# Optimization experiments

Hardware: AMD Instinct MI355X
Metric: run time of the kernel (lower is better)

## Reference

```python
import jax, jax.numpy as jnp
import numpy as np
from jax import lax

B, T, V, E, H = 256, 512, 128, 64, 256


def lstm_cell(x, h, c, Wih, Whh, bih, bhh):
    # PyTorch gate order: i, f, g, o
    gates = x @ Wih.T + h @ Whh.T + bih + bhh
    i, f, g, o = jnp.split(gates, 4, axis=-1)
    c_new = jax.nn.sigmoid(f) * c + jax.nn.sigmoid(i) * jnp.tanh(g)
    h_new = jax.nn.sigmoid(o) * jnp.tanh(c_new)
    return h_new, c_new


def setup_inputs() -> dict:
    key = jax.random.key(0)
    ks = jax.random.split(key, 16)
    s = 0.05
    emb = jax.random.normal(ks[1], (V, E), jnp.float32) * s
    emb = emb.at[0].set(0.0)  # padding_idx=0
    return {
        "x": jax.random.randint(ks[0], (B, T), 0, V),
        "emb": emb,
        "Wih_e": jax.random.normal(ks[2], (4 * H, E), jnp.float32) * s,
        "Whh_e": jax.random.normal(ks[3], (4 * H, H), jnp.float32) * s,
        "bih_e": jax.random.normal(ks[4], (4 * H,), jnp.float32) * s,
        "bhh_e": jax.random.normal(ks[5], (4 * H,), jnp.float32) * s,
        "Wq": jax.random.normal(ks[6], (H, H), jnp.float32) * s,
        "Wk": jax.random.normal(ks[7], (H, H), jnp.float32) * s,
        "v": jax.random.normal(ks[8], (H,), jnp.float32) * s,
        "Wih_d": jax.random.normal(ks[9], (4 * H, E + H), jnp.float32) * s,
        "Whh_d": jax.random.normal(ks[10], (4 * H, H), jnp.float32) * s,
        "bih_d": jax.random.normal(ks[11], (4 * H,), jnp.float32) * s,
        "bhh_d": jax.random.normal(ks[12], (4 * H,), jnp.float32) * s,
        "Wfc": jax.random.normal(ks[13], (V, H), jnp.float32) * s,
        "bfc": jax.random.normal(ks[14], (V,), jnp.float32) * s,
    }


def reference(x, emb, Wih_e, Whh_e, bih_e, bhh_e, Wq, Wk, v,
              Wih_d, Whh_d, bih_d, bhh_d, Wfc, bfc):
    Bx = x.shape[0]
    embedded = emb[x]                          # (B, T, E)  (dropout in eval mode = identity)
    emb_tbE = embedded.transpose(1, 0, 2)      # (T, B, E)

    # ---- Encoder LSTM ----
    h0 = jnp.zeros((Bx, H), embedded.dtype)
    c0 = jnp.zeros((Bx, H), embedded.dtype)

    def enc_step(carry, x_t):
        h, c = carry
        h, c = lstm_cell(x_t, h, c, Wih_e, Whh_e, bih_e, bhh_e)
        return (h, c), h

    (h_n, c_n), enc_seq = lax.scan(enc_step, (h0, c0), emb_tbE)
    enc_out = enc_seq.transpose(1, 0, 2)       # (B, T, H)

    # ---- Attention precompute ----
    keys_proj = enc_out @ Wk.T                 # (B, T, H)
    pad_mask = (x == 0)                        # (B, T)

    # ---- Decoder loop (teacher forcing) ----
    def dec_step(carry, emb_t):
        h, c = carry
        q = h @ Wq.T                                        # (B, H)
        energy = jnp.tanh(q[:, None, :] + keys_proj) @ v    # (B, T)
        energy = jnp.where(pad_mask, -1e9, energy)
        w = jax.nn.softmax(energy, axis=-1)
        context = jnp.einsum('bt,bth->bh', w, enc_out)      # (B, H)
        dec_in = jnp.concatenate([emb_t, context], axis=-1)  # (B, E+H)
        h, c = lstm_cell(dec_in, h, c, Wih_d, Whh_d, bih_d, bhh_d)
        return (h, c), h

    (h_f, c_f), dec_seq = lax.scan(dec_step, (h_n, c_n), emb_tbE)
    logits = dec_seq.transpose(1, 0, 2) @ Wfc.T + bfc       # (B, T, V)
    return logits, h_f, c_f
```

## Files before the change

kernel.cpp:

```cpp
#include <hip/hip_runtime.h>
#include <hip/hip_bf16.h>
#include <stdint.h>

#define NB 256
#define NT 512
#define NV 128
#define NE 64
#define NH 256

typedef __fp16 h2t __attribute__((ext_vector_type(2)));

__device__ __forceinline__ float lo_bf(unsigned u){ return __uint_as_float(u << 16); }
__device__ __forceinline__ float hi_bf(unsigned u){ return __uint_as_float(u & 0xffff0000u); }
__device__ __forceinline__ unsigned short f2us(float f){
  unsigned u = __float_as_uint(f);
  unsigned r = u + 0x7fffu + ((u >> 16) & 1u);
  return (unsigned short)(r >> 16);
}
__device__ __forceinline__ float sigm(float x){
  return __builtin_amdgcn_rcpf(1.f + __expf(-x));
}
__device__ __forceinline__ float ftanh(float xx){
  float a = fabsf(xx);
  a = fminf(a, 9.f);
  float e = __expf(2.f * a);
  float r = __builtin_amdgcn_rcpf(e + 1.f);
  float t = (e - 1.f) * r;
  return copysignf(t, xx);
}
__device__ __forceinline__ unsigned pkf16(float a, float b){
  h2t h = __builtin_amdgcn_cvt_pkrtz(a, b);
  unsigned u; __builtin_memcpy(&u, &h, 4); return u;
}
__device__ __forceinline__ float fdot2(unsigned a, unsigned b, float c){
#if __has_builtin(__builtin_amdgcn_fdot2)
  h2t A, B; __builtin_memcpy(&A, &a, 4); __builtin_memcpy(&B, &b, 4);
  return __builtin_amdgcn_fdot2(A, B, c, false);
#else
  h2t A, B; __builtin_memcpy(&A, &a, 4); __builtin_memcpy(&B, &b, 4);
  return c + (float)A.x*(float)B.x + (float)A.y*(float)B.y;
#endif
}

__global__ __launch_bounds__(256, 1)
void prep_kernel(const float* __restrict__ Wq, const float* __restrict__ Wfc,
                 const float* __restrict__ Wihd, const float* __restrict__ Whhd,
                 const float* __restrict__ Wihe, const float* __restrict__ Whhe,
                 const float* __restrict__ Wk,
                 unsigned* __restrict__ Wq4, unsigned* __restrict__ Wfc4,
                 unsigned* __restrict__ Wihd4, unsigned* __restrict__ Whhd4,
                 unsigned* __restrict__ Wihe4, unsigned* __restrict__ Whhe4,
                 unsigned* __restrict__ Wke4)
{
  const int blk = blockIdx.x, tid = threadIdx.x;
  if (blk < 64){
    int k2p = blk;
    #pragma unroll
    for (int l = 0; l < 2; ++l){
      int i = l*256 + tid, c = i>>1, j = i&1, k = 4*k2p + 2*j;
      Wq4[k2p*512 + i] = pkf16(Wq[c*256 + k], Wq[c*256 + k + 1]);
    }
  } else if (blk < 128){
    int k2p = blk - 64;
    int c = tid>>1, j = tid&1, k = 4*k2p + 2*j;
    Wfc4[k2p*256 + tid] = pkf16(Wfc[c*256 + k], Wfc[c*256 + k + 1]);
  } else if (blk < 208){
    int k2p = blk - 128;
    #pragma unroll
    for (int l = 0; l < 8; ++l){
      int i = l*256 + tid, g = i>>1, j = i&1, k = 4*k2p + 2*j;
      Wihd4[(size_t)k2p*2048 + i] = pkf16(Wihd[g*320 + k], Wihd[g*320 + k + 1]);
    }
  } else if (blk < 272){
    int k2p = blk - 208;
    #pragma unroll
    for (int l = 0; l < 8; ++l){
      int i = l*256 + tid, g = i>>1, j = i&1, k = 4*k2p + 2*j;
      Whhd4[(size_t)k2p*2048 + i] = pkf16(Whhd[g*256 + k], Whhd[g*256 + k + 1]);
    }
  } else if (blk < 288){
    int k2p = blk - 272;
    #pragma unroll
    for (int l = 0; l < 8; ++l){
      int i = l*256 + tid, g = i>>1, j = i&1, k = 4*k2p + 2*j;
      Wihe4[(size_t)k2p*2048 + i] = pkf16(Wihe[g*64 + k], Wihe[g*64 + k + 1]);
    }
  } else if (blk < 352){
    int k2p = blk - 288;
    #pragma unroll
    for (int l = 0; l < 8; ++l){
      int i = l*256 + tid, g = i>>1, j = i&1, k = 4*k2p + 2*j;
      Whhe4[(size_t)k2p*2048 + i] = pkf16(Whhe[g*256 + k], Whhe[g*256 + k + 1]);
    }
  } else {
    int k2p = blk - 352;
    #pragma unroll
    for (int l = 0; l < 2; ++l){
      int i = l*256 + tid, c = i>>1, j = i&1, k = 4*k2p + 2*j;
      Wke4[k2p*512 + i] = pkf16(Wk[c*256 + k], Wk[c*256 + k + 1]);
    }
  }
}

__global__ __launch_bounds__(256, 1)
void tr_kernel(const unsigned short* __restrict__ keys_n, unsigned short* __restrict__ keys_t)
{
  __shared__ unsigned short tile[64][68];
  const int blk = blockIdx.x, tid = threadIdx.x;
  const int b  = blk >> 5;
  const int tt = (blk >> 2) & 7;
  const int hh = blk & 3;
  const int t0 = tt*64, h0 = hh*64;

  #pragma unroll
  for (int i = 0; i < 4; ++i){
    int idx = tid + i*256;
    int t = idx >> 4, h4 = (idx & 15)*4;
    uint2 u = *(const uint2*)(keys_n + ((size_t)b*NT + t0 + t)*NH + h0 + h4);
    *(uint2*)&tile[t][h4] = u;
  }
  __syncthreads();
  #pragma unroll
  for (int i = 0; i < 4; ++i){
    int idx = tid + i*256;
    int h = idx >> 4, t4 = (idx & 15)*4;
    unsigned short a = tile[t4+0][h], bb = tile[t4+1][h], cc = tile[t4+2][h], dd = tile[t4+3][h];
    uint2 u; u.x = (unsigned)a | ((unsigned)bb << 16); u.y = (unsigned)cc | ((unsigned)dd << 16);
    *(uint2*)(keys_t + ((size_t)b*NH + h0 + h)*NT + t0 + t4) = u;
  }
}

__global__ __launch_bounds__(1024, 1)
void enc_kernel(const int* __restrict__ x, const float* __restrict__ emb,
                const unsigned* __restrict__ Wihe4, const unsigned* __restrict__ Whhe4,
                const float* __restrict__ bih, const float* __restrict__ bhh,
                const unsigned* __restrict__ Wke4,
                unsigned short* __restrict__ enc_out, unsigned short* __restrict__ keys_n,
                float* __restrict__ g_h, float* __restrict__ g_c)
{
  const int tid = threadIdx.x;
  const int b0  = blockIdx.x * 2;

  __shared__ unsigned sH2[2][128];
  __shared__ unsigned sXe2[2][32];
  __shared__ float sG[2][1024];
  __shared__ float sBias[1024];
  __shared__ float sKP[1024];
  __shared__ uint8_t sXi[2][512];

  sBias[tid] = bih[tid] + bhh[tid];
  { int r = tid >> 9; sXi[r][tid & 511] = (uint8_t)x[(b0 + r)*NT + (tid & 511)]; }
  if (tid < 256) sH2[tid>>7][tid&127] = 0u;
  __syncthreads();
  if (tid < 64){
    int r = tid>>5, p = tid&31, idx = sXi[r][0];
    sXe2[r][p] = pkf16(emb[idx*NE + 2*p], emb[idx*NE + 2*p + 1]);
  }
  float creg = 0.f, hl = 0.f;
  __syncthreads();

  for (int t = 0; t < NT; ++t){
    {
      const int g = tid;
      float a0 = sBias[g], a1 = a0;
      const unsigned* Wi = Wihe4 + g*2;
      #pragma unroll 4
      for (int p = 0; p < 16; ++p){
        uint2 w = *(const uint2*)(Wi + (size_t)p*2048);
        a0 = fdot2(sXe2[0][2*p], w.x, a0); a0 = fdot2(sXe2[0][2*p+1], w.y, a0);
        a1 = fdot2(sXe2[1][2*p], w.x, a1); a1 = fdot2(sXe2[1][2*p+1], w.y, a1);
      }
      const unsigned* Wh = Whhe4 + g*2;
      #pragma unroll 4
      for (int p = 0; p < 64; ++p){
        uint2 w = *(const uint2*)(Wh + (size_t)p*2048);
        a0 = fdot2(sH2[0][2*p], w.x, a0); a0 = fdot2(sH2[0][2*p+1], w.y, a0);
        a1 = fdot2(sH2[1][2*p], w.x, a1); a1 = fdot2(sH2[1][2*p+1], w.y, a1);
      }
      sG[0][g] = a0; sG[1][g] = a1;
    }
    if (t > 0){
      const int r = tid>>9, half = (tid>>8)&1, c = tid&255;
      float kp = 0.f;
      const unsigned* Wk4 = Wke4 + c*2;
      #pragma unroll 4
      for (int p = 0; p < 32; ++p){
        int k2p = half*32 + p;
        uint2 w = *(const uint2*)(Wk4 + k2p*512);
        kp = fdot2(sH2[r][2*k2p], w.x, kp);
        kp = fdot2(sH2[r][2*k2p+1], w.y, kp);
      }
      sKP[tid] = kp;
    }
    __syncthreads();
    if (tid < 512){
      const int r = tid>>8, cc = tid&255;
      float gi = sigm (sG[r][cc]);
      float gf = sigm (sG[r][256+cc]);
      float gg = ftanh(sG[r][512+cc]);
      float go = sigm (sG[r][768+cc]);
      float cn = gf*creg + gi*gg;
      float hn = go*ftanh(cn);
      creg = cn; hl = hn;
      enc_out[((size_t)(b0+r)*NT + t)*NH + cc] = f2us(hn);
      float hb = __shfl_down(hn, 1, 64);
      if (!(cc & 1)) sH2[r][cc>>1] = pkf16(hn, hb);
      if (tid < 64 && (t+1) < NT){
        int r2 = tid>>5, p = tid&31, idx = sXi[r2][t+1];
        sXe2[r2][p] = pkf16(emb[idx*NE + 2*p], emb[idx*NE + 2*p + 1]);
      }
    } else if (t > 0){
      const int r = (tid>>8)&1, c = tid&255;
      float kv = sKP[(r<<9) + c] + sKP[(r<<9) + 256 + c];
      keys_n[((size_t)(b0+r)*NT + (t-1))*NH + c] = f2us(kv);
    }
    __syncthreads();
  }
  {
    const int r = tid>>9, half = (tid>>8)&1, c = tid&255;
    float kp = 0.f;
    const unsigned* Wk4 = Wke4 + c*2;
    #pragma unroll 4
    for (int p = 0; p < 32; ++p){
      int k2p = half*32 + p;
      uint2 w = *(const uint2*)(Wk4 + k2p*512);
      kp = fdot2(sH2[r][2*k2p], w.x, kp);
      kp = fdot2(sH2[r][2*k2p+1], w.y, kp);
    }
    sKP[tid] = kp;
  }
  __syncthreads();
  if (tid >= 512){
    const int r = (tid>>8)&1, c = tid&255;
    float kv = sKP[(r<<9) + c] + sKP[(r<<9) + 256 + c];
    keys_n[((size_t)(b0+r)*NT + (NT-1))*NH + c] = f2us(kv);
  } else {
    const int r = tid>>8, cc = tid&255;
    g_h[(b0+r)*NH + cc] = hl;
    g_c[(b0+r)*NH + cc] = creg;
  }
}

__global__ __launch_bounds__(1024, 1)
void dec_kernel(const int* __restrict__ x, const float* __restrict__ emb,
                const unsigned* __restrict__ Wq4, const float* __restrict__ vvec,
                const unsigned* __restrict__ Wihd4, const unsigned* __restrict__ Whhd4,
                const float* __restrict__ bih, const float* __restrict__ bhh,
                const unsigned short* __restrict__ enc_out, const unsigned short* __restrict__ keys_t,
                const float* __restrict__ g_h, const float* __restrict__ g_c,
                unsigned* __restrict__ h2_hist, float* __restrict__ out_h, float* __restrict__ out_c)
{
  const int tid = threadIdx.x;
  const int b   = blockIdx.x;

  extern __shared__ unsigned short sKpin[];

  __shared__ float sTMP[4096];
  __shared__ float sWp[512];
  __shared__ float sRed[8];
  __shared__ float sQ2[256];
  __shared__ unsigned sH2[128];
  __shared__ unsigned sCtx2[128];
  __shared__ unsigned sXe2[32];
  __shared__ float sG[1024];
  __shared__ float sBiasD[1024];
  __shared__ float sVm2[256];
  __shared__ float sVs[8];
  __shared__ uint8_t sXi[512];

  sBiasD[tid] = bih[tid] + bhh[tid];
  if (tid < 256) sVm2[tid] = -2.f * vvec[tid];
  if (tid < 512) sXi[tid] = (uint8_t)x[b*NT + tid];
  if (tid < 128) sH2[tid] = pkf16(g_h[b*NH + 2*tid], g_h[b*NH + 2*tid + 1]);
  if (tid < 8){
    float s = 0.f;
    #pragma unroll
    for (int j = 0; j < 32; ++j) s += vvec[tid*32 + j];
    sVs[tid] = s;
  }
  {
    const unsigned* src = (const unsigned*)(keys_t + (size_t)b*NH*NT);
    unsigned* dst = (unsigned*)sKpin;
    #pragma unroll
    for (int i = 0; i < 24; ++i) dst[tid + i*1024] = src[tid + i*1024];
  }
  float creg = (tid < 256) ? g_c[b*NH + tid] : 0.f;
  float hl = 0.f;
  const float CLN = 2.885390081777927f;
  __syncthreads();

  for (int t = 0; t < NT; ++t){
    uint2 pf[16];
    {
      const int c = tid & 255, kq = tid >> 8;
      float a = 0.f;
      const unsigned* Wp = Wq4 + c*2;
      #pragma unroll 4
      for (int p = 0; p < 16; ++p){
        int k2p = kq*16 + p;
        uint2 w = *(const uint2*)(Wp + k2p*512);
        a = fdot2(sH2[2*k2p], w.x, a);
        a = fdot2(sH2[2*k2p+1], w.y, a);
      }
      sTMP[kq*256 + c] = a;
    }
    __syncthreads();
    if (tid < 256){
      float qv = sTMP[tid] + sTMP[256 + tid] + sTMP[512 + tid] + sTMP[768 + tid];
      sQ2[tid] = CLN * qv;
    } else if (tid < 288){
      int p = tid - 256, idx = sXi[t];
      sXe2[p] = pkf16(emb[idx*NE + 2*p], emb[idx*NE + 2*p + 1]);
    }
    __syncthreads();
    {
      const int sc = tid >> 6, kc = tid & 63;
      const unsigned short* ep = enc_out + ((size_t)b*NT + sc*32)*NH + kc*4;
      #pragma unroll
      for (int ss = 0; ss < 16; ++ss) pf[ss] = *(const uint2*)(ep + (size_t)ss*NH);
    }
    {
      const int kh = tid >> 7, sp = tid & 127;
      float e0 = sVs[kh], e1 = e0, e2 = e0, e3 = e0;
      if (kh < 3){
        const unsigned short* ktp = sKpin + (size_t)(kh*32)*NT + sp*4;
        #pragma unroll 4
        for (int kk = 0; kk < 32; ++kk){
          uint2 u = *(const uint2*)(ktp + (size_t)kk*NT);
          float q2 = sQ2[kh*32 + kk];
          float vm = sVm2[kh*32 + kk];
          float r0 = __builtin_amdgcn_rcpf(1.f + exp2f(fmaf(CLN, lo_bf(u.x), q2)));
          float r1 = __builtin_amdgcn_rcpf(1.f + exp2f(fmaf(CLN, hi_bf(u.x), q2)));
          float r2 = __builtin_amdgcn_rcpf(1.f + exp2f(fmaf(CLN, lo_bf(u.y), q2)));
          float r3 = __builtin_amdgcn_rcpf(1.f + exp2f(fmaf(CLN, hi_bf(u.y), q2)));
          e0 = fmaf(vm, r0, e0); e1 = fmaf(vm, r1, e1);
          e2 = fmaf(vm, r2, e2); e3 = fmaf(vm, r3, e3);
        }
      } else {
        const unsigned short* ktp = keys_t + ((size_t)b*NH + kh*32)*NT + sp*4;
        #pragma unroll 4
        for (int kk = 0; kk < 32; ++kk){
          uint2 u = *(const uint2*)(ktp + (size_t)kk*NT);
          float q2 = sQ2[kh*32 + kk];
          float vm = sVm2[kh*32 + kk];
          float r0 = __builtin_amdgcn_rcpf(1.f + exp2f(fmaf(CLN, lo_bf(u.x), q2)));
          float r1 = __builtin_amdgcn_rcpf(1.f + exp2f(fmaf(CLN, hi_bf(u.x), q2)));
          float r2 = __builtin_amdgcn_rcpf(1.f + exp2f(fmaf(CLN, lo_bf(u.y), q2)));
          float r3 = __builtin_amdgcn_rcpf(1.f + exp2f(fmaf(CLN, hi_bf(u.y), q2)));
          e0 = fmaf(vm, r0, e0); e1 = fmaf(vm, r1, e1);
          e2 = fmaf(vm, r2, e2); e3 = fmaf(vm, r3, e3);
        }
      }
      *(float4*)(sTMP + kh*512 + sp*4) = make_float4(e0,e1,e2,e3);
    }
    __syncthreads();
    if (tid < 512){
      float e = sTMP[tid]      + sTMP[512+tid]  + sTMP[1024+tid] + sTMP[1536+tid]
              + sTMP[2048+tid] + sTMP[2560+tid] + sTMP[3072+tid] + sTMP[3584+tid];
      float w = (sXi[tid] == 0) ? 0.f : __expf(e);
      sWp[tid] = w;
      float s = w;
      #pragma unroll
      for (int off = 32; off > 0; off >>= 1) s += __shfl_down(s, off, 64);
      if ((tid & 63) == 0) sRed[tid >> 6] = s;
    }
    __syncthreads();
    {
      const int sc = tid >> 6;
      const int kc = tid & 63;
      const unsigned short* ep = enc_out + ((size_t)b*NT + sc*32)*NH + kc*4;
      float a0=0.f, a1=0.f, a2=0.f, a3=0.f;
      #pragma unroll
      for (int ss = 0; ss < 16; ++ss){
        float w = sWp[sc*32 + ss];
        uint2 u = pf[ss];
        a0 += w*lo_bf(u.x); a1 += w*hi_bf(u.x);
        a2 += w*lo_bf(u.y); a3 += w*hi_bf(u.y);
      }
      #pragma unroll 4
      for (int ss = 16; ss < 32; ++ss){
        float w = sWp[sc*32 + ss];
        uint2 u = *(const uint2*)(ep + (size_t)ss*NH);
        a0 += w*lo_bf(u.x); a1 += w*hi_bf(u.x);
        a2 += w*lo_bf(u.y); a3 += w*hi_bf(u.y);
      }
      *(float4*)(sTMP + sc*256 + kc*4) = make_float4(a0,a1,a2,a3);
    }
    __syncthreads();
    if (tid < 256){
      float den = sRed[0]+sRed[1]+sRed[2]+sRed[3]+sRed[4]+sRed[5]+sRed[6]+sRed[7];
      float rden = (den > 0.f) ? (1.f/den) : 0.f;
      float cs = 0.f;
      #pragma unroll
      for (int p = 0; p < 16; ++p) cs += sTMP[p*256 + tid];
      float cv = cs * rden;
      float cb = __shfl_down(cv, 1, 64);
      if (!(tid & 1)) sCtx2[tid>>1] = pkf16(cv, cb);
    }
    __syncthreads();
    {
      const int g = tid;
      float a = sBiasD[g];
      const unsigned* Wi = Wihd4 + g*2;
      #pragma unroll 4
      for (int p = 0; p < 16; ++p){
        uint2 w = *(const uint2*)(Wi + (size_t)p*2048);
        a = fdot2(sXe2[2*p], w.x, a); a = fdot2(sXe2[2*p+1], w.y, a);
      }
      #pragma unroll 4
      for (int p = 0; p < 64; ++p){
        uint2 w = *(const uint2*)(Wi + (size_t)(16+p)*2048);
        a = fdot2(sCtx2[2*p], w.x, a); a = fdot2(sCtx2[2*p+1], w.y, a);
      }
      const unsigned* Wh = Whhd4 + g*2;
      #pragma unroll 4
      for (int p = 0; p < 64; ++p){
        uint2 w = *(const uint2*)(Wh + (size_t)p*2048);
        a = fdot2(sH2[2*p], w.x, a); a = fdot2(sH2[2*p+1], w.y, a);
      }
      sG[g] = a;
    }
    __syncthreads();
    if (tid < 256){
      float gi = sigm (sG[tid]);
      float gf = sigm (sG[256 + tid]);
      float gg = ftanh(sG[512 + tid]);
      float go = sigm (sG[768 + tid]);
      float cn = gf*creg + gi*gg;
      float hn = go*ftanh(cn);
      creg = cn; hl = hn;
      float hb = __shfl_down(hn, 1, 64);
      if (!(tid & 1)){
        unsigned hp = pkf16(hn, hb);
        sH2[tid>>1] = hp;
        h2_hist[((size_t)b*NT + t)*128 + (tid>>1)] = hp;
      }
    }
    __syncthreads();
  }

  if (tid < 256){
    out_h[b*NH + tid] = hl;
    out_c[b*NH + tid] = creg;
  }
}

__global__ __launch_bounds__(256, 1)
void fc_kernel(const unsigned* __restrict__ h2_hist, const unsigned* __restrict__ Wfc4,
               const float* __restrict__ bfc, float* __restrict__ logits)
{
  __shared__ unsigned sHH[1024];
  const int tid = threadIdx.x;
  const size_t row0 = (size_t)blockIdx.x * 8;
  #pragma unroll
  for (int l = 0; l < 4; ++l) sHH[l*256 + tid] = h2_hist[row0*128 + l*256 + tid];
  __syncthreads();
  const int r = tid >> 7, v = tid & 127;
  float bv = bfc[v];
  float a0 = bv, a1 = bv, a2 = bv, a3 = bv;
  const unsigned* Wp = Wfc4 + v*2;
  #pragma unroll 4
  for (int k2p = 0; k2p < 64; ++k2p){
    uint2 w = *(const uint2*)(Wp + k2p*256);
    int k2 = 2*k2p;
    a0 = fdot2(sHH[(r  )*128 + k2], w.x, a0); a0 = fdot2(sHH[(r  )*128 + k2+1], w.y, a0);
    a1 = fdot2(sHH[(r+2)*128 + k2], w.x, a1); a1 = fdot2(sHH[(r+2)*128 + k2+1], w.y, a1);
    a2 = fdot2(sHH[(r+4)*128 + k2], w.x, a2); a2 = fdot2(sHH[(r+4)*128 + k2+1], w.y, a2);
    a3 = fdot2(sHH[(r+6)*128 + k2], w.x, a3); a3 = fdot2(sHH[(r+6)*128 + k2+1], w.y, a3);
  }
  logits[(row0 + r    )*NV + v] = a0;
  logits[(row0 + r + 2)*NV + v] = a1;
  logits[(row0 + r + 4)*NV + v] = a2;
  logits[(row0 + r + 6)*NV + v] = a3;
}

extern "C" void kernel_launch(void* const* d_in, const int* in_sizes, int n_in,
                              void* d_out, int out_size, void* d_ws, size_t ws_size,
                              hipStream_t stream)
{
  (void)in_sizes; (void)n_in; (void)out_size; (void)ws_size;
  const int*   x    = (const int*)  d_in[0];
  const float* emb  = (const float*)d_in[1];
  const float* Wihe = (const float*)d_in[2];
  const float* Whhe = (const float*)d_in[3];
  const float* bihe = (const float*)d_in[4];
  const float* bhhe = (const float*)d_in[5];
  const float* Wq   = (const float*)d_in[6];
  const float* Wk   = (const float*)d_in[7];
  const float* vv   = (const float*)d_in[8];
  const float* Wihd = (const float*)d_in[9];
  const float* Whhd = (const float*)d_in[10];
  const float* bihd = (const float*)d_in[11];
  const float* bhhd = (const float*)d_in[12];
  const float* Wfc  = (const float*)d_in[13];
  const float* bfc  = (const float*)d_in[14];

  char* ws = (char*)d_ws;
  const size_t M64 = 67108864;
  unsigned short* enc   = (unsigned short*)(ws);
  unsigned short* keysn = (unsigned short*)(ws + M64);
  unsigned short* keyst = (unsigned short*)(ws + 2*M64);
  unsigned* h2_hist     = (unsigned*)(ws + M64);
  float* g_h = (float*)(ws + 3*M64);
  float* g_c = g_h + NB*NH;
  unsigned* Wq4   = (unsigned*)(g_c + NB*NH);
  unsigned* Wfc4  = Wq4   + 64*512;
  unsigned* Wihd4 = Wfc4  + 64*256;
  unsigned* Whhd4 = Wihd4 + 80*2048;
  unsigned* Wihe4 = Whhd4 + 64*2048;
  unsigned* Whhe4 = Wihe4 + 16*2048;
  unsigned* Wke4  = Whhe4 + 64*2048;

  float* out_logits = (float*)d_out;
  float* out_h = out_logits + (size_t)NB*NT*NV;
  float* out_c = out_h + NB*NH;

  const int dynLds = 96 * 512 * 2;
  static int attrSet = 0;
  if (!attrSet){
    hipFuncSetAttribute(reinterpret_cast<const void*>(dec_kernel),
                        hipFuncAttributeMaxDynamicSharedMemorySize, dynLds);
    attrSet = 1;
  }

  prep_kernel<<<dim3(416), dim3(256), 0, stream>>>(
      Wq, Wfc, Wihd, Whhd, Wihe, Whhe, Wk,
      Wq4, Wfc4, Wihd4, Whhd4, Wihe4, Whhe4, Wke4);
  enc_kernel<<<dim3(128), dim3(1024), 0, stream>>>(
      x, emb, Wihe4, Whhe4, bihe, bhhe, Wke4, enc, keysn, g_h, g_c);
  tr_kernel<<<dim3(8192), dim3(256), 0, stream>>>(keysn, keyst);
  dec_kernel<<<dim3(256), dim3(1024), dynLds, stream>>>(
      x, emb, Wq4, vv, Wihd4, Whhd4, bihd, bhhd,
      enc, keyst, g_h, g_c, h2_hist, out_h, out_c);
  fc_kernel<<<dim3(16384), dim3(256), 0, stream>>>(h2_hist, Wfc4, bfc, out_logits);
}
```

Baseline: 28.57 ms.

## Balance attention key rows across all warps mixing LDS and global reads

Before, three of the eight thread groups read 32 key rows each from shared memory while the other five read 32 rows each from global memory, so the global-bound groups ran longer. Now every group handles 12 LDS-resident rows and 20 global rows, and the per-group v-sum partition is changed to match. The register prefetch of enc_out ahead of the energy phase is also removed, with all 32 rows loaded in the context loop. This trades load overlap for lower register pressure and an even per-warp load.

Measured after the change: 25.47 ms. 10.8% less time.

```diff
diff --git a/kernel.cpp b/kernel.cpp
--- a/kernel.cpp
+++ b/kernel.cpp
@@ -275,7 +275,9 @@
   if (tid < 8){
     float s = 0.f;
     #pragma unroll
-    for (int j = 0; j < 32; ++j) s += vvec[tid*32 + j];
+    for (int j = 0; j < 12; ++j) s += vvec[tid*12 + j];
+    #pragma unroll
+    for (int j = 0; j < 20; ++j) s += vvec[96 + tid*20 + j];
     sVs[tid] = s;
   }
   {
@@ -290,7 +292,6 @@
   __syncthreads();
 
   for (int t = 0; t < NT; ++t){
-    uint2 pf[16];
     {
       const int c = tid & 255, kq = tid >> 8;
       float a = 0.f;
@@ -314,42 +315,35 @@
     }
     __syncthreads();
     {
-      const int sc = tid >> 6, kc = tid & 63;
-      const unsigned short* ep = enc_out + ((size_t)b*NT + sc*32)*NH + kc*4;
-      #pragma unroll
-      for (int ss = 0; ss < 16; ++ss) pf[ss] = *(const uint2*)(ep + (size_t)ss*NH);
-    }
-    {
       const int kh = tid >> 7, sp = tid & 127;
       float e0 = sVs[kh], e1 = e0, e2 = e0, e3 = e0;
-      if (kh < 3){
-        const unsigned short* ktp = sKpin + (size_t)(kh*32)*NT + sp*4;
-        #pragma unroll 4
-        for (int kk = 0; kk < 32; ++kk){
-          uint2 u = *(const uint2*)(ktp + (size_t)kk*NT);
-          float q2 = sQ2[kh*32 + kk];
-          float vm = sVm2[kh*32 + kk];
-          float r0 = __builtin_amdgcn_rcpf(1.f + exp2f(fmaf(CLN, lo_bf(u.x), q2)));
-          float r1 = __builtin_amdgcn_rcpf(1.f + exp2f(fmaf(CLN, hi_bf(u.x), q2)));
-          float r2 = __builtin_amdgcn_rcpf(1.f + exp2f(fmaf(CLN, lo_bf(u.y), q2)));
-          float r3 = __builtin_amdgcn_rcpf(1.f + exp2f(fmaf(CLN, hi_bf(u.y), q2)));
-          e0 = fmaf(vm, r0, e0); e1 = fmaf(vm, r1, e1);
-          e2 = fmaf(vm, r2, e2); e3 = fmaf(vm, r3, e3);
-        }
-      } else {
-        const unsigned short* ktp = keys_t + ((size_t)b*NH + kh*32)*NT + sp*4;
-        #pragma unroll 4
-        for (int kk = 0; kk < 32; ++kk){
-          uint2 u = *(const uint2*)(ktp + (size_t)kk*NT);
-          float q2 = sQ2[kh*32 + kk];
-          float vm = sVm2[kh*32 + kk];
-          float r0 = __builtin_amdgcn_rcpf(1.f + exp2f(fmaf(CLN, lo_bf(u.x), q2)));
-          float r1 = __builtin_amdgcn_rcpf(1.f + exp2f(fmaf(CLN, hi_bf(u.x), q2)));
-          float r2 = __builtin_amdgcn_rcpf(1.f + exp2f(fmaf(CLN, lo_bf(u.y), q2)));
-          float r3 = __builtin_amdgcn_rcpf(1.f + exp2f(fmaf(CLN, hi_bf(u.y), q2)));
-          e0 = fmaf(vm, r0, e0); e1 = fmaf(vm, r1, e1);
-          e2 = fmaf(vm, r2, e2); e3 = fmaf(vm, r3, e3);
-        }
+      const unsigned short* ktg = keys_t + ((size_t)b*NH + 96 + kh*20)*NT + sp*4;
+      #pragma unroll 4
+      for (int j = 0; j < 20; ++j){
+        uint2 u = *(const uint2*)(ktg + (size_t)j*NT);
+        int ka = 96 + kh*20 + j;
+        float q2 = sQ2[ka];
+        float vm = sVm2[ka];
+        float r0 = __builtin_amdgcn_rcpf(1.f + exp2f(fmaf(CLN, lo_bf(u.x), q2)));
+        float r1 = __builtin_amdgcn_rcpf(1.f + exp2f(fmaf(CLN, hi_bf(u.x), q2)));
+        float r2 = __builtin_amdgcn_rcpf(1.f + exp2f(fmaf(CLN, lo_bf(u.y), q2)));
+        float r3 = __builtin_amdgcn_rcpf(1.f + exp2f(fmaf(CLN, hi_bf(u.y), q2)));
+        e0 = fmaf(vm, r0, e0); e1 = fmaf(vm, r1, e1);
+        e2 = fmaf(vm, r2, e2); e3 = fmaf(vm, r3, e3);
+      }
+      const unsigned short* ktl = sKpin + (size_t)(kh*12)*NT + sp*4;
+      #pragma unroll 4
+      for (int j = 0; j < 12; ++j){
+        uint2 u = *(const uint2*)(ktl + (size_t)j*NT);
+        int ka = kh*12 + j;
+        float q2 = sQ2[ka];
+        float vm = sVm2[ka];
+        float r0 = __builtin_amdgcn_rcpf(1.f + exp2f(fmaf(CLN, lo_bf(u.x), q2)));
+        float r1 = __builtin_amdgcn_rcpf(1.f + exp2f(fmaf(CLN, hi_bf(u.x), q2)));
+        float r2 = __builtin_amdgcn_rcpf(1.f + exp2f(fmaf(CLN, lo_bf(u.y), q2)));
+        float r3 = __builtin_amdgcn_rcpf(1.f + exp2f(fmaf(CLN, hi_bf(u.y), q2)));
+        e0 = fmaf(vm, r0, e0); e1 = fmaf(vm, r1, e1);
+        e2 = fmaf(vm, r2, e2); e3 = fmaf(vm, r3, e3);
       }
       *(float4*)(sTMP + kh*512 + sp*4) = make_float4(e0,e1,e2,e3);
     }
@@ -370,15 +364,8 @@
       const int kc = tid & 63;
       const unsigned short* ep = enc_out + ((size_t)b*NT + sc*32)*NH + kc*4;
       float a0=0.f, a1=0.f, a2=0.f, a3=0.f;
-      #pragma unroll
-      for (int ss = 0; ss < 16; ++ss){
-        float w = sWp[sc*32 + ss];
-        uint2 u = pf[ss];
-        a0 += w*lo_bf(u.x); a1 += w*hi_bf(u.x);
-        a2 += w*lo_bf(u.y); a3 += w*hi_bf(u.y);
-      }
-      #pragma unroll 4
-      for (int ss = 16; ss < 32; ++ss){
+      #pragma unroll 8
+      for (int ss = 0; ss < 32; ++ss){
         float w = sWp[sc*32 + ss];
         uint2 u = *(const uint2*)(ep + (size_t)ss*NH);
         a0 += w*lo_bf(u.x); a1 += w*hi_bf(u.x);
```
